# Kernel tuning notes

Measured on AMD Instinct MI355X. Metric: run time of the kernel, lower is better.

## Reference

```python
import jax, jax.numpy as jnp
import numpy as np

B, IN_DIM, OUT_DIM = 4096, 8192, 8192

# Each of the 16 gates op_i(a,b) is affine in (1, a, b, a*b).
# Rows: [const, coef_a, coef_b, coef_ab] for gate i = 0..15.
GATE_COEF = np.array([
    [0.,  0.,  0.,  0.],   # 0: zeros
    [0.,  0.,  0.,  1.],   # 1: a*b
    [0.,  1.,  0., -1.],   # 2: a - a*b
    [0.,  1.,  0.,  0.],   # 3: a
    [0.,  0.,  1., -1.],   # 4: b - a*b
    [0.,  0.,  1.,  0.],   # 5: b
    [0.,  1.,  1., -2.],   # 6: a + b - 2ab (xor)
    [0.,  1.,  1., -1.],   # 7: a + b - ab (or)
    [1., -1., -1.,  1.],   # 8: 1 - (a + b - ab)
    [1., -1., -1.,  2.],   # 9: 1 - (a + b - 2ab)
    [1.,  0., -1.,  0.],   # 10: 1 - b
    [1.,  0., -1.,  1.],   # 11: 1 - b + ab
    [1., -1.,  0.,  0.],   # 12: 1 - a
    [1., -1.,  0.,  1.],   # 13: 1 - a + ab
    [1.,  0.,  0., -1.],   # 14: 1 - ab
    [1.,  0.,  0.,  0.],   # 15: ones
], dtype=np.float32)


def setup_inputs() -> dict:
    key = jax.random.key(0)
    k1, k2, k3, k4 = jax.random.split(key, 4)
    x = jax.random.uniform(k1, (B, IN_DIM), dtype=jnp.float32)
    weights = jax.random.normal(k2, (OUT_DIM, 16), dtype=jnp.float32)
    idx0 = jax.random.randint(k3, (OUT_DIM,), 0, IN_DIM)
    idx1 = jax.random.randint(k4, (OUT_DIM,), 0, IN_DIM)
    return {"x": x, "weights": weights, "idx0": idx0, "idx1": idx1}


def reference(x, weights, idx0, idx1):
    # training path: soft mixture over 16 gates
    p = jax.nn.softmax(weights, axis=-1)          # [out_dim, 16]
    c = p @ jnp.asarray(GATE_COEF)                # [out_dim, 4]: sum_i p_i * op_i collapsed
    a = x[:, idx0]                                # [B, out_dim]
    b = x[:, idx1]                                # [B, out_dim]
    return c[:, 0] + c[:, 1] * a + c[:, 2] * b + c[:, 3] * (a * b)
```

## Files before the change

kernel.cpp:

```cpp
#include <hip/hip_runtime.h>

#define IN_DIM 8192
#define OUT_DIM 8192
#define NROWS 4096
#define THREADS 512
#define RPB 2
#define JITERS (OUT_DIM / (THREADS * 4))

typedef float v4f __attribute__((ext_vector_type(4)));

__device__ __constant__ float GATE_COEF[16][4] = {
    {0.f, 0.f, 0.f, 0.f}, {0.f, 0.f, 0.f, 1.f}, {0.f, 1.f, 0.f, -1.f}, {0.f, 1.f, 0.f, 0.f},
    {0.f, 0.f, 1.f, -1.f}, {0.f, 0.f, 1.f, 0.f}, {0.f, 1.f, 1.f, -2.f}, {0.f, 1.f, 1.f, -1.f},
    {1.f, -1.f, -1.f, 1.f}, {1.f, -1.f, -1.f, 2.f}, {1.f, 0.f, -1.f, 0.f}, {1.f, 0.f, -1.f, 1.f},
    {1.f, -1.f, 0.f, 0.f}, {1.f, -1.f, 0.f, 1.f}, {1.f, 0.f, 0.f, -1.f}, {1.f, 0.f, 0.f, 0.f}};

__global__ __launch_bounds__(256) void compute_c_kernel(const float* __restrict__ w,
                                                        float* __restrict__ cp) {
    int j = blockIdx.x * blockDim.x + threadIdx.x;
    if (j >= OUT_DIM) return;
    const float4* wv = (const float4*)(w + (size_t)j * 16);
    float4 w0 = wv[0], w1 = wv[1], w2 = wv[2], w3 = wv[3];
    float wa[16] = {w0.x, w0.y, w0.z, w0.w, w1.x, w1.y, w1.z, w1.w,
                    w2.x, w2.y, w2.z, w2.w, w3.x, w3.y, w3.z, w3.w};
    float m = wa[0];
#pragma unroll
    for (int k = 1; k < 16; ++k) m = fmaxf(m, wa[k]);
    float p[16];
    float s = 0.f;
#pragma unroll
    for (int k = 0; k < 16; ++k) {
        p[k] = __expf(wa[k] - m);
        s += p[k];
    }
    float inv = 1.f / s;
    float c0 = 0.f, c1 = 0.f, c2 = 0.f, c3 = 0.f;
#pragma unroll
    for (int k = 0; k < 16; ++k) {
        c0 = fmaf(p[k], GATE_COEF[k][0], c0);
        c1 = fmaf(p[k], GATE_COEF[k][1], c1);
        c2 = fmaf(p[k], GATE_COEF[k][2], c2);
        c3 = fmaf(p[k], GATE_COEF[k][3], c3);
    }
    cp[j] = c0 * inv;
    cp[j + OUT_DIM] = c1 * inv;
    cp[j + 2 * OUT_DIM] = c2 * inv;
    cp[j + 3 * OUT_DIM] = c3 * inv;
}

__global__ __launch_bounds__(THREADS, 4) void gate_kernel(const float* __restrict__ x,
                                                          const float* __restrict__ cp,
                                                          const int* __restrict__ idx0,
                                                          const int* __restrict__ idx1,
                                                          float* __restrict__ out) {
    __shared__ float rows[RPB * IN_DIM];
    const int r0 = blockIdx.x * RPB;
    const int tid = threadIdx.x;

    const v4f* xr0 = (const v4f*)(x + (size_t)r0 * IN_DIM);
    const v4f* xr1 = (const v4f*)(x + (size_t)(r0 + 1) * IN_DIM);
    v4f* rv0 = (v4f*)rows;
    v4f* rv1 = (v4f*)(rows + IN_DIM);
    v4f st[8];
#pragma unroll
    for (int t = 0; t < 4; ++t) st[t] = __builtin_nontemporal_load(xr0 + tid + t * THREADS);
#pragma unroll
    for (int t = 0; t < 4; ++t) st[4 + t] = __builtin_nontemporal_load(xr1 + tid + t * THREADS);

    const int j0 = tid * 4;
    int4 pi0 = *(const int4*)(idx0 + j0);
    int4 pi1 = *(const int4*)(idx1 + j0);

#pragma unroll
    for (int t = 0; t < 4; ++t) rv0[tid + t * THREADS] = st[t];
#pragma unroll
    for (int t = 0; t < 4; ++t) rv1[tid + t * THREADS] = st[4 + t];
    __syncthreads();

    const float* __restrict__ c0p = cp;
    const float* __restrict__ c1p = cp + OUT_DIM;
    const float* __restrict__ c2p = cp + 2 * OUT_DIM;
    const float* __restrict__ c3p = cp + 3 * OUT_DIM;
    float* o0 = out + (size_t)r0 * OUT_DIM;
    float* o1 = out + (size_t)(r0 + 1) * OUT_DIM;

#pragma unroll
    for (int k = 0; k < JITERS; ++k) {
        const int j = k * (THREADS * 4) + tid * 4;
        const int4 i0 = pi0;
        const int4 i1 = pi1;
        if (k < JITERS - 1) {
            const int jn = j + THREADS * 4;
            pi0 = *(const int4*)(idx0 + jn);
            pi1 = *(const int4*)(idx1 + jn);
        }
        const v4f c0v = *(const v4f*)(c0p + j);
        const v4f c1v = *(const v4f*)(c1p + j);
        const v4f c2v = *(const v4f*)(c2p + j);
        const v4f c3v = *(const v4f*)(c3p + j);
        v4f a0, b0, a1, b1;
        a0.x = rows[i0.x]; a0.y = rows[i0.y]; a0.z = rows[i0.z]; a0.w = rows[i0.w];
        b0.x = rows[i1.x]; b0.y = rows[i1.y]; b0.z = rows[i1.z]; b0.w = rows[i1.w];
        a1.x = rows[IN_DIM + i0.x]; a1.y = rows[IN_DIM + i0.y];
        a1.z = rows[IN_DIM + i0.z]; a1.w = rows[IN_DIM + i0.w];
        b1.x = rows[IN_DIM + i1.x]; b1.y = rows[IN_DIM + i1.y];
        b1.z = rows[IN_DIM + i1.z]; b1.w = rows[IN_DIM + i1.w];

        const v4f r0v = c0v + c1v * a0 + c2v * b0 + c3v * (a0 * b0);
        const v4f r1v = c0v + c1v * a1 + c2v * b1 + c3v * (a1 * b1);
        *(v4f*)(o0 + j) = r0v;
        *(v4f*)(o1 + j) = r1v;
    }
}

extern "C" void kernel_launch(void* const* d_in, const int* in_sizes, int n_in,
                              void* d_out, int out_size, void* d_ws, size_t ws_size,
                              hipStream_t stream) {
    const float* x = (const float*)d_in[0];
    const float* weights = (const float*)d_in[1];
    const int* idx0 = (const int*)d_in[2];
    const int* idx1 = (const int*)d_in[3];
    float* out = (float*)d_out;
    float* cp = (float*)d_ws;

    compute_c_kernel<<<OUT_DIM / 256, 256, 0, stream>>>(weights, cp);
    gate_kernel<<<NROWS / RPB, THREADS, 0, stream>>>(x, cp, idx0, idx1, out);
}
```

Baseline: 234.5 us.

## Load x rows directly into LDS, double block size, prefetch gate coefficients

The gate kernel now stages the two input rows into shared memory with direct global-to-LDS loads, instead of loading through registers and storing to LDS. Each block now runs 1024 threads with an occupancy hint of 8. The coefficient vectors are prefetched one iteration ahead, alongside the index prefetch. The aim is to cut register staging and load latency in the prologue and main loop. The aggressive launch-bounds hint with 64KB of LDS per block may constrain registers without actually allowing more blocks per CU.

Result: no change. 237.6 us (+1.3%).

```diff
diff --git a/kernel.cpp b/kernel.cpp
--- a/kernel.cpp
+++ b/kernel.cpp
@@ -3,8 +3,9 @@
 #define IN_DIM 8192
 #define OUT_DIM 8192
 #define NROWS 4096
-#define THREADS 512
+#define THREADS 1024
 #define RPB 2
+#define NBLK (NROWS / RPB)
 #define JITERS (OUT_DIM / (THREADS * 4))
 
 typedef float v4f __attribute__((ext_vector_type(4)));
@@ -48,39 +49,41 @@
     cp[j + 3 * OUT_DIM] = c3 * inv;
 }
 
-__global__ __launch_bounds__(THREADS, 4) void gate_kernel(const float* __restrict__ x,
+__global__ __launch_bounds__(THREADS, 8) void gate_kernel(const float* __restrict__ x,
                                                           const float* __restrict__ cp,
                                                           const int* __restrict__ idx0,
                                                           const int* __restrict__ idx1,
                                                           float* __restrict__ out) {
-    __shared__ float rows[RPB * IN_DIM];
+    __shared__ __align__(16) float rows[RPB * IN_DIM];
     const int r0 = blockIdx.x * RPB;
     const int tid = threadIdx.x;
 
-    const v4f* xr0 = (const v4f*)(x + (size_t)r0 * IN_DIM);
-    const v4f* xr1 = (const v4f*)(x + (size_t)(r0 + 1) * IN_DIM);
-    v4f* rv0 = (v4f*)rows;
-    v4f* rv1 = (v4f*)(rows + IN_DIM);
-    v4f st[8];
+    {
+        const float* xr = x + (size_t)r0 * IN_DIM;
 #pragma unroll
-    for (int t = 0; t < 4; ++t) st[t] = __builtin_nontemporal_load(xr0 + tid + t * THREADS);
-#pragma unroll
-    for (int t = 0; t < 4; ++t) st[4 + t] = __builtin_nontemporal_load(xr1 + tid + t * THREADS);
-
-    const int j0 = tid * 4;
-    int4 pi0 = *(const int4*)(idx0 + j0);
-    int4 pi1 = *(const int4*)(idx1 + j0);
-
-#pragma unroll
-    for (int t = 0; t < 4; ++t) rv0[tid + t * THREADS] = st[t];
-#pragma unroll
-    for (int t = 0; t < 4; ++t) rv1[tid + t * THREADS] = st[4 + t];
-    __syncthreads();
+        for (int t = 0; t < 2 * RPB; ++t) {
+            const int off = tid * 4 + t * (THREADS * 4);
+            __builtin_amdgcn_global_load_lds(
+                (const __attribute__((address_space(1))) void*)(xr + off),
+                (__attribute__((address_space(3))) void*)(rows + off), 16, 0, 0);
+        }
+    }
 
     const float* __restrict__ c0p = cp;
     const float* __restrict__ c1p = cp + OUT_DIM;
     const float* __restrict__ c2p = cp + 2 * OUT_DIM;
     const float* __restrict__ c3p = cp + 3 * OUT_DIM;
+
+    const int j0 = tid * 4;
+    int4 pi0 = *(const int4*)(idx0 + j0);
+    int4 pi1 = *(const int4*)(idx1 + j0);
+    v4f pc0 = *(const v4f*)(c0p + j0);
+    v4f pc1 = *(const v4f*)(c1p + j0);
+    v4f pc2 = *(const v4f*)(c2p + j0);
+    v4f pc3 = *(const v4f*)(c3p + j0);
+
+    __syncthreads();
+
     float* o0 = out + (size_t)r0 * OUT_DIM;
     float* o1 = out + (size_t)(r0 + 1) * OUT_DIM;
 
@@ -89,15 +92,16 @@
         const int j = k * (THREADS * 4) + tid * 4;
         const int4 i0 = pi0;
         const int4 i1 = pi1;
+        const v4f c0v = pc0, c1v = pc1, c2v = pc2, c3v = pc3;
         if (k < JITERS - 1) {
             const int jn = j + THREADS * 4;
             pi0 = *(const int4*)(idx0 + jn);
             pi1 = *(const int4*)(idx1 + jn);
+            pc0 = *(const v4f*)(c0p + jn);
+            pc1 = *(const v4f*)(c1p + jn);
+            pc2 = *(const v4f*)(c2p + jn);
+            pc3 = *(const v4f*)(c3p + jn);
         }
-        const v4f c0v = *(const v4f*)(c0p + j);
-        const v4f c1v = *(const v4f*)(c1p + j);
-        const v4f c2v = *(const v4f*)(c2p + j);
-        const v4f c3v = *(const v4f*)(c3p + j);
         v4f a0, b0, a1, b1;
         a0.x = rows[i0.x]; a0.y = rows[i0.y]; a0.z = rows[i0.z]; a0.w = rows[i0.w];
         b0.x = rows[i1.x]; b0.y = rows[i1.y]; b0.z = rows[i1.z]; b0.w = rows[i1.w];
@@ -124,5 +128,5 @@
     float* cp = (float*)d_ws;
 
     compute_c_kernel<<<OUT_DIM / 256, 256, 0, stream>>>(weights, cp);
-    gate_kernel<<<NROWS / RPB, THREADS, 0, stream>>>(x, cp, idx0, idx1, out);
+    gate_kernel<<<NBLK, THREADS, 0, stream>>>(x, cp, idx0, idx1, out);
 }
```
